# Kernel optimization log

Measured on AMD Instinct MI355X. Metric: run time of the kernel, lower is better.

## Reference

```python
import jax, jax.numpy as jnp
import numpy as np

DIM = 2048
NUM_HEADS = 16
HEAD_DIM = DIM // NUM_HEADS
HIDDEN = 4 * DIM
EPS = 1e-6


def rmsnorm(x, w):
    # Faithful to source: weight * (x * dim**-0.5 / sqrt(mean(x^2) + eps))
    scale = DIM ** -0.5
    norm = jnp.sqrt(jnp.mean(x * x, axis=-1, keepdims=True) + EPS)
    return w * (x * scale / norm)


def setup_inputs() -> dict:
    key = jax.random.key(0)
    ks = jax.random.split(key, 10)
    def init(k, shape, fan_in):
        return jax.random.normal(k, shape, dtype=jnp.float32) * (fan_in ** -0.5)
    return {
        "x": jax.random.normal(ks[0], (2, 2048, DIM), dtype=jnp.float32),
        "norm1_w": jnp.ones((DIM,), dtype=jnp.float32),
        "wq": init(ks[1], (DIM, DIM), DIM),
        "wk": init(ks[2], (HEAD_DIM, DIM), DIM),
        "wv": init(ks[3], (HEAD_DIM, DIM), DIM),
        "wo": init(ks[4], (DIM, DIM), DIM),
        "norm2_w": jnp.ones((DIM,), dtype=jnp.float32),
        "w1": init(ks[5], (HIDDEN, DIM), DIM),
        "w2": init(ks[6], (DIM, HIDDEN), HIDDEN),
        "w3": init(ks[7], (HIDDEN, DIM), DIM),
    }


def reference(x, norm1_w, wq, wk, wv, wo, norm2_w, w1, w2, w3):
    B, S, _ = x.shape
    # --- Multi-Query Attention (pre-norm) ---
    h = rmsnorm(x, norm1_w)
    q = h @ wq.T                                  # [B,S,D]
    k = h @ wk.T                                  # [B,S,hd] (shared across heads)
    v = h @ wv.T                                  # [B,S,hd]
    q = q.reshape(B, S, NUM_HEADS, HEAD_DIM)
    # scores: q @ k^T / sqrt(hd); k is broadcast (repeated) across heads
    scores = jnp.einsum('bshd,btd->bhst', q, k) / (HEAD_DIM ** 0.5)  # [B,H,S,S]
    probs = jax.nn.softmax(scores, axis=-1)
    attn = jnp.einsum('bhst,btd->bshd', probs, v).reshape(B, S, DIM)
    x = x + attn @ wo.T
    # --- SwiGLU FFN (pre-norm) ---
    h = rmsnorm(x, norm2_w)
    ffn = (jax.nn.silu(h @ w1.T) * (h @ w3.T)) @ w2.T
    return x + ffn
```

## Files before the change

kernel.cpp:

```cpp
#include <hip/hip_runtime.h>
#include <hip/hip_bf16.h>

typedef __attribute__((ext_vector_type(4))) float f32x4;
typedef __attribute__((ext_vector_type(8))) short s16x8;
typedef __attribute__((ext_vector_type(4))) short s16x4;
typedef __attribute__((ext_vector_type(2))) short s16x2;

#define MFMA_BF16 __builtin_amdgcn_mfma_f32_16x16x32_bf16

__device__ inline short f2bf(float f) {
  unsigned u = __float_as_uint(f);
  u = (u + 0x7FFFu + ((u >> 16) & 1u)) >> 16;
  return (short)u;
}
__device__ inline float bf2f(short s) {
  return __uint_as_float(((unsigned)(unsigned short)s) << 16);
}

#define DPPF(x, ctrl) __int_as_float(__builtin_amdgcn_update_dpp( \
    __float_as_int(x), __float_as_int(x), ctrl, 0xF, 0xF, false))
__device__ inline float rowmax16(float x) {
  x = fmaxf(x, DPPF(x, 0xB1));
  x = fmaxf(x, DPPF(x, 0x4E));
  x = fmaxf(x, DPPF(x, 0x124));
  x = fmaxf(x, DPPF(x, 0x128));
  return x;
}
__device__ inline float rowsum16(float x) {
  x += DPPF(x, 0xB1);
  x += DPPF(x, 0x4E);
  x += DPPF(x, 0x124);
  x += DPPF(x, 0x128);
  return x;
}

__global__ __launch_bounds__(256) void cvt_kernel(
    const float* __restrict__ in, short* __restrict__ out, int n, float scale)
{
  int idx = (blockIdx.x * 256 + threadIdx.x) * 8;
  if (idx >= n) return;
  f32x4 a = *(const f32x4*)(in + idx);
  f32x4 b = *(const f32x4*)(in + idx + 4);
  s16x8 o;
  #pragma unroll
  for (int j = 0; j < 4; ++j) { o[j] = f2bf(a[j] * scale); o[4 + j] = f2bf(b[j] * scale); }
  *(s16x8*)(out + idx) = o;
}

__global__ __launch_bounds__(256) void rmsnorm_kernel(
    const float* __restrict__ x, const float* __restrict__ w, short* __restrict__ out)
{
  size_t row = blockIdx.x;
  const float* xr = x + row * 2048;
  int base = threadIdx.x * 8;
  f32x4 a = *(const f32x4*)(xr + base);
  f32x4 b = *(const f32x4*)(xr + base + 4);
  float ss = a[0]*a[0] + a[1]*a[1] + a[2]*a[2] + a[3]*a[3]
           + b[0]*b[0] + b[1]*b[1] + b[2]*b[2] + b[3]*b[3];
  #pragma unroll
  for (int off = 1; off < 64; off <<= 1) ss += __shfl_xor(ss, off, 64);
  __shared__ float red[4];
  if ((threadIdx.x & 63) == 0) red[threadIdx.x >> 6] = ss;
  __syncthreads();
  float tot = red[0] + red[1] + red[2] + red[3];
  float rn = rsqrtf(tot * (1.0f / 2048.0f) + 1e-6f) * 0.022097086912079608f;
  f32x4 wa = *(const f32x4*)(w + base);
  f32x4 wb = *(const f32x4*)(w + base + 4);
  s16x8 o;
  #pragma unroll
  for (int j = 0; j < 4; ++j) {
    o[j]     = f2bf(a[j] * wa[j] * rn);
    o[4 + j] = f2bf(b[j] * wb[j] * rn);
  }
  *(s16x8*)(out + row * 2048 + base) = o;
}

template <int MODE>
__global__ __launch_bounds__(256, 2) void gemm_bt_kernel(
    const short* __restrict__ A, const short* __restrict__ B,
    void* __restrict__ Cv, const float* __restrict__ resid,
    int M, int N, int K)
{
  __shared__ short As[128 * 32];
  __shared__ short Bs[128 * 32];
  int tid = threadIdx.x;
  int lane = tid & 63;
  int w = tid >> 6;
  int r = lane & 15, g = lane >> 4;
  int wr = w >> 1, wc = w & 1;
  size_t row0 = (size_t)blockIdx.y * 128;
  size_t col0 = (size_t)blockIdx.x * 128;

  f32x4 acc[4][4];
  #pragma unroll
  for (int i = 0; i < 4; ++i)
    #pragma unroll
    for (int j = 0; j < 4; ++j) acc[i][j] = (f32x4){0.f, 0.f, 0.f, 0.f};

  const short* Ablk = A + row0 * K;
  const short* Bblk = B + col0 * K;
  int arow = tid >> 2;
  int akk = (tid & 3) << 3;

  for (int k0 = 0; k0 < K; k0 += 32) {
    #pragma unroll
    for (int i = 0; i < 2; ++i) {
      int chunk = i * 256 + tid;
      int rr = i * 64 + arow;
      __builtin_amdgcn_global_load_lds(
          (const __attribute__((address_space(1))) unsigned int*)(Ablk + (size_t)rr * K + k0 + akk),
          (__attribute__((address_space(3))) unsigned int*)(&As[chunk * 8]), 16, 0, 0);
      __builtin_amdgcn_global_load_lds(
          (const __attribute__((address_space(1))) unsigned int*)(Bblk + (size_t)rr * K + k0 + akk),
          (__attribute__((address_space(3))) unsigned int*)(&Bs[chunk * 8]), 16, 0, 0);
    }
    __syncthreads();
    s16x8 af[4], bfr[4];
    #pragma unroll
    for (int mm = 0; mm < 4; ++mm)
      af[mm] = *(const s16x8*)(&As[(wr * 64 + mm * 16 + r) * 32 + g * 8]);
    #pragma unroll
    for (int nn = 0; nn < 4; ++nn)
      bfr[nn] = *(const s16x8*)(&Bs[(wc * 64 + nn * 16 + r) * 32 + g * 8]);
    #pragma unroll
    for (int mm = 0; mm < 4; ++mm)
      #pragma unroll
      for (int nn = 0; nn < 4; ++nn)
        acc[mm][nn] = MFMA_BF16(af[mm], bfr[nn], acc[mm][nn], 0, 0, 0);
    __syncthreads();
  }

  #pragma unroll
  for (int mm = 0; mm < 4; ++mm) {
    #pragma unroll
    for (int nn = 0; nn < 4; ++nn) {
      #pragma unroll
      for (int j = 0; j < 4; ++j) {
        size_t rr = row0 + wr * 64 + mm * 16 + g * 4 + j;
        size_t cc = col0 + wc * 64 + nn * 16 + r;
        size_t idx = rr * (size_t)N + cc;
        if constexpr (MODE == 0) {
          ((short*)Cv)[idx] = f2bf(acc[mm][nn][j]);
        } else if constexpr (MODE == 1) {
          ((float*)Cv)[idx] = acc[mm][nn][j] + resid[idx];
        } else {
          short* gp = (short*)Cv;
          float gv = bf2f(gp[idx]);
          float sg = gv / (1.0f + __expf(-gv));
          gp[idx] = f2bf(sg * acc[mm][nn][j]);
        }
      }
    }
  }
}


#define STAGEA2(T)                                                             \
  _Pragma("unroll")                                                            \
  for (int i = 0; i < 4; ++i) {                                                \
    int lc = i * 512 + tid;                                                    \
    int rw = lc >> 3, ch = lc & 7;                                             \
    __builtin_amdgcn_global_load_lds(                                          \
        (const __attribute__((address_space(1))) unsigned int*)                \
            (Ablk + (size_t)rw * K + (T) * 64 + ((ch ^ (rw & 7)) << 3)),       \
        (__attribute__((address_space(3))) unsigned int*)                      \
            (&As[(T) & 1][lc * 8]), 16, 0, 0);                                 \
  }

#define STAGEB2(T)                                                             \
  _Pragma("unroll")                                                            \
  for (int i = 0; i < BLOADS2; ++i) {                                          \
    int lc = i * 512 + tid;                                                    \
    int rw = lc >> 3, ch = lc & 7;                                             \
    __builtin_amdgcn_global_load_lds(                                          \
        (const __attribute__((address_space(1))) unsigned int*)                \
            (Bblk + (size_t)rw * K + (T) * 64 + ((ch ^ (rw & 7)) << 3)),       \
        (__attribute__((address_space(3))) unsigned int*)                      \
            (&Bs[(T) & 1][lc * 8]), 16, 0, 0);                                 \
  }

#define LDALL(D, KS)                                                           \
  _Pragma("unroll")                                                            \
  for (int mi = 0; mi < 8; ++mi) {                                             \
    int rowa = wr * 128 + mi * 16 + r;                                         \
    aR[mi] = *(const s16x8*)(&As[D][rowa * 64 + ((((KS) * 4 + g) ^ (rowa & 7)) << 3)]); \
  }                                                                            \
  _Pragma("unroll")                                                            \
  for (int ni = 0; ni < NREP; ++ni) {                                          \
    int rowb = wc * WN + ni * 16 + r;                                          \
    bR[ni] = *(const s16x8*)(&Bs[D][rowb * 64 + ((((KS) * 4 + g) ^ (rowb & 7)) << 3)]); \
  }

#define MFALL                                                                  \
  __builtin_amdgcn_s_setprio(1);                                               \
  _Pragma("unroll")                                                            \
  for (int mi = 0; mi < 8; ++mi)                                               \
    _Pragma("unroll")                                                          \
    for (int ni = 0; ni < NREP; ++ni)                                          \
      acc[mi][ni] = MFMA_BF16(aR[mi], bR[ni], acc[mi][ni], 0, 0, 0);           \
  __builtin_amdgcn_s_setprio(0);

#define BAR __builtin_amdgcn_s_barrier()
#define VM0 asm volatile("s_waitcnt vmcnt(0)" ::: "memory")

template <int BN, int MODE>
__global__ __launch_bounds__(512, 2) void gemm2p_kernel(
    const short* __restrict__ A, const short* __restrict__ B,
    void* __restrict__ Cv, const float* __restrict__ resid,
    int M, int N, int K)
{
  constexpr int BLOADS2 = BN / 64;
  constexpr int WN = BN / 4;
  constexpr int NREP = WN / 16;
  __shared__ short As[2][256 * 64];
  __shared__ short Bs[2][BN * 64];

  int tid = threadIdx.x;
  int lane = tid & 63;
  int w = tid >> 6;
  int r = lane & 15, g = lane >> 4;
  int wr = w >> 2, wc = w & 3;

  int nwg = gridDim.x * gridDim.y;
  int orig = blockIdx.y * gridDim.x + blockIdx.x;
  int swz = (orig & 7) * (nwg >> 3) + (orig >> 3);
  int bx = swz % gridDim.x, by = swz / gridDim.x;
  size_t row0 = (size_t)by * 256;
  size_t col0 = (size_t)bx * BN;

  const short* Ablk = A + row0 * K;
  const short* Bblk = B + col0 * K;

  f32x4 acc[8][NREP];
  #pragma unroll
  for (int i = 0; i < 8; ++i)
    #pragma unroll
    for (int j = 0; j < NREP; ++j) acc[i][j] = (f32x4){0.f, 0.f, 0.f, 0.f};

  s16x8 aR[8], bR[NREP];
  int NT = K >> 6;

  STAGEA2(0); STAGEB2(0);
  VM0;
  BAR;

  for (int t = 0; t < NT; ++t) {
    int d = t & 1;
    bool nl = (t < NT - 1);
    if (nl) { STAGEA2(t + 1); STAGEB2(t + 1); }
    LDALL(d, 0);
    BAR;
    MFALL;
    BAR;
    LDALL(d, 1);
    VM0;
    BAR;
    MFALL;
    BAR;
  }

  #pragma unroll
  for (int mi = 0; mi < 8; ++mi) {
    #pragma unroll
    for (int ni = 0; ni < NREP; ++ni) {
      #pragma unroll
      for (int j = 0; j < 4; ++j) {
        size_t rr = row0 + wr * 128 + mi * 16 + g * 4 + j;
        size_t cc = col0 + wc * WN + ni * 16 + r;
        size_t idx = rr * (size_t)N + cc;
        if constexpr (MODE == 0) {
          ((short*)Cv)[idx] = f2bf(acc[mi][ni][j]);
        } else if constexpr (MODE == 1) {
          ((float*)Cv)[idx] = acc[mi][ni][j] + resid[idx];
        } else {
          short* gp = (short*)Cv;
          float gv = bf2f(gp[idx]);
          float sg = gv / (1.0f + __expf(-gv));
          gp[idx] = f2bf(sg * acc[mi][ni][j]);
        }
      }
    }
  }
}

__global__ __launch_bounds__(256) void transpose_v_kernel(
    const short* __restrict__ kv, short* __restrict__ vt)
{
  __shared__ short t[64][65];
  int b = blockIdx.z;
  int s0 = blockIdx.x * 64;
  int d0 = blockIdx.y * 64;
  int tid = threadIdx.x;
  #pragma unroll
  for (int i = 0; i < 16; ++i) {
    int e = i * 256 + tid;
    int sr = e >> 6, dc = e & 63;
    t[sr][dc] = kv[(size_t)(b * 2048 + s0 + sr) * 256 + 128 + d0 + dc];
  }
  __syncthreads();
  #pragma unroll
  for (int i = 0; i < 16; ++i) {
    int e = i * 256 + tid;
    int dr = e >> 6, sc = e & 63;
    vt[(size_t)b * 128 * 2048 + (size_t)(d0 + dr) * 2048 + s0 + sc] = t[sc][dr];
  }
}

__global__ __launch_bounds__(256, 2) void attn_kernel(
    const short* __restrict__ q, const short* __restrict__ kv,
    const short* __restrict__ vt, short* __restrict__ out)
{
  const int S = 2048;
  int tid = threadIdx.x;
  int w = tid >> 6;
  int lane = tid & 63;
  int r = lane & 15, g = lane >> 4;
  int h = blockIdx.y, b = blockIdx.z;
  int qrow0 = blockIdx.x * 128 + w * 32;

  __shared__ short Ks[2][4096];
  __shared__ short Vs[2][4096];
  __shared__ short Ps[4][32][40];

  const short* kvsrc = kv + (size_t)b * S * 256;
  const short* vsrc  = vt + (size_t)b * 128 * S;

  const short* qbase = q + ((size_t)(b * S + qrow0 + r)) * 2048 + h * 128;
  s16x8 qa[2][4];
  #pragma unroll
  for (int gq = 0; gq < 2; ++gq)
    #pragma unroll
    for (int dc = 0; dc < 4; ++dc)
      qa[gq][dc] = *(const s16x8*)(qbase + gq * 16 * 2048 + dc * 32 + g * 8);

  f32x4 o[2][8];
  #pragma unroll
  for (int gq = 0; gq < 2; ++gq)
    #pragma unroll
    for (int dt = 0; dt < 8; ++dt) o[gq][dt] = (f32x4){0.f, 0.f, 0.f, 0.f};
  float m[2][4], l[2][4];
  #pragma unroll
  for (int gq = 0; gq < 2; ++gq)
    #pragma unroll
    for (int j = 0; j < 4; ++j) { m[gq][j] = -1e30f; l[gq][j] = 0.f; }

#define STAGE(KVT, BSEL)                                                        \
  {                                                                             \
    int kv0s = (KVT) * 32;                                                      \
    _Pragma("unroll")                                                           \
    for (int i = 0; i < 2; ++i) {                                               \
      int c = w * 64 + lane + i * 256;                                          \
      int krow = c >> 4, kcp = c & 15;                                          \
      __builtin_amdgcn_global_load_lds(                                         \
          (const __attribute__((address_space(1))) unsigned int*)               \
              (kvsrc + (size_t)(kv0s + krow) * 256 + ((kcp ^ (krow & 7)) << 3)),\
          (__attribute__((address_space(3))) unsigned int*)(&Ks[BSEL][c * 8]),  \
          16, 0, 0);                                                            \
      int vrow = c >> 2, vcp = c & 3;                                           \
      __builtin_amdgcn_global_load_lds(                                         \
          (const __attribute__((address_space(1))) unsigned int*)               \
              (vsrc + (size_t)vrow * S + kv0s + ((vcp ^ (vrow & 3)) << 3)),     \
          (__attribute__((address_space(3))) unsigned int*)(&Vs[BSEL][c * 8]),  \
          16, 0, 0);                                                            \
    }                                                                           \
  }

  STAGE(0, 0);
  __syncthreads();

  for (int it = 0; it < 64; ++it) {
    int cur = it & 1;
    if (it < 63) STAGE(it + 1, cur ^ 1);

    s16x8 kc0[4], kc1[4], vb[8];
    #pragma unroll
    for (int dc = 0; dc < 4; ++dc) {
      kc0[dc] = *(const s16x8*)(&Ks[cur][r * 128 + (((dc * 4 + g) ^ (r & 7)) << 3)]);
      kc1[dc] = *(const s16x8*)(&Ks[cur][(16 + r) * 128 + (((dc * 4 + g) ^ (r & 7)) << 3)]);
    }
    #pragma unroll
    for (int dt = 0; dt < 8; ++dt)
      vb[dt] = *(const s16x8*)(&Vs[cur][(dt * 16 + r) * 32 + ((g ^ (r & 3)) << 3)]);

    f32x4 sc0[2], sc1[2];
    #pragma unroll
    for (int gq = 0; gq < 2; ++gq) { sc0[gq] = (f32x4){0.f,0.f,0.f,0.f}; sc1[gq] = (f32x4){0.f,0.f,0.f,0.f}; }
    __builtin_amdgcn_s_setprio(1);
    #pragma unroll
    for (int dc = 0; dc < 4; ++dc) {
      #pragma unroll
      for (int gq = 0; gq < 2; ++gq) {
        sc0[gq] = MFMA_BF16(qa[gq][dc], kc0[dc], sc0[gq], 0, 0, 0);
        sc1[gq] = MFMA_BF16(qa[gq][dc], kc1[dc], sc1[gq], 0, 0, 0);
      }
    }
    __builtin_amdgcn_s_setprio(0);

    float p0[2][4], p1[2][4];
    #pragma unroll
    for (int gq = 0; gq < 2; ++gq) {
      float mx[4];
      #pragma unroll
      for (int j = 0; j < 4; ++j) mx[j] = rowmax16(fmaxf(sc0[gq][j], sc1[gq][j]));
      bool nd = (mx[0] > m[gq][0] + 8.f) | (mx[1] > m[gq][1] + 8.f)
              | (mx[2] > m[gq][2] + 8.f) | (mx[3] > m[gq][3] + 8.f);
      if (__any(nd)) {
        #pragma unroll
        for (int j = 0; j < 4; ++j) {
          float mn = fmaxf(m[gq][j], mx[j]);
          float alpha = __expf(m[gq][j] - mn);
          m[gq][j] = mn;
          l[gq][j] *= alpha;
          #pragma unroll
          for (int dt = 0; dt < 8; ++dt) o[gq][dt][j] *= alpha;
        }
      }
      #pragma unroll
      for (int j = 0; j < 4; ++j) {
        p0[gq][j] = __expf(sc0[gq][j] - m[gq][j]);
        p1[gq][j] = __expf(sc1[gq][j] - m[gq][j]);
        l[gq][j] += p0[gq][j] + p1[gq][j];
      }
      #pragma unroll
      for (int j = 0; j < 4; ++j) {
        Ps[w][gq * 16 + g * 4 + j][r]      = f2bf(p0[gq][j]);
        Ps[w][gq * 16 + g * 4 + j][16 + r] = f2bf(p1[gq][j]);
      }
    }
    asm volatile("s_waitcnt lgkmcnt(0)" ::: "memory");
    __builtin_amdgcn_sched_barrier(0);
    s16x8 pa0 = *(const s16x8*)(&Ps[w][r][g * 8]);
    s16x8 pa1 = *(const s16x8*)(&Ps[w][16 + r][g * 8]);
    __builtin_amdgcn_s_setprio(1);
    #pragma unroll
    for (int dt = 0; dt < 8; ++dt) {
      o[0][dt] = MFMA_BF16(pa0, vb[dt], o[0][dt], 0, 0, 0);
      o[1][dt] = MFMA_BF16(pa1, vb[dt], o[1][dt], 0, 0, 0);
    }
    __builtin_amdgcn_s_setprio(0);
    __syncthreads();
  }

  #pragma unroll
  for (int gq = 0; gq < 2; ++gq) {
    float linv[4];
    #pragma unroll
    for (int j = 0; j < 4; ++j) linv[j] = 1.0f / rowsum16(l[gq][j]);
    short* ob = out + ((size_t)(b * S + qrow0 + gq * 16)) * 2048 + h * 128;
    #pragma unroll
    for (int dt = 0; dt < 8; ++dt)
      #pragma unroll
      for (int j = 0; j < 4; ++j)
        ob[(size_t)(g * 4 + j) * 2048 + dt * 16 + r] = f2bf(o[gq][dt][j] * linv[j]);
  }
#undef STAGE
}

extern "C" void kernel_launch(void* const* d_in, const int* in_sizes, int n_in,
                              void* d_out, int out_size, void* d_ws, size_t ws_size,
                              hipStream_t stream) {
  const float* x   = (const float*)d_in[0];
  const float* n1w = (const float*)d_in[1];
  const float* wq  = (const float*)d_in[2];
  const float* wk  = (const float*)d_in[3];
  const float* wv  = (const float*)d_in[4];
  const float* wo  = (const float*)d_in[5];
  const float* n2w = (const float*)d_in[6];
  const float* w1  = (const float*)d_in[7];
  const float* w2  = (const float*)d_in[8];
  const float* w3  = (const float*)d_in[9];
  float* out = (float*)d_out;
  char* ws = (char*)d_ws;
  const size_t MB = 1ull << 20;
  short* wqb  = (short*)(ws);
  short* wob  = (short*)(ws + 8 * MB);
  short* w1b  = (short*)(ws + 16 * MB);
  short* w2b  = (short*)(ws + 48 * MB);
  short* w3b  = (short*)(ws + 80 * MB);
  short* wkvb = (short*)(ws + 112 * MB);
  short* h1   = (short*)(ws + 113 * MB);
  short* gbuf = (short*)(ws + 129 * MB);
  short* qb   = (short*)(ws + 129 * MB);
  short* kvb  = (short*)(ws + 145 * MB);
  short* vtb  = (short*)(ws + 147 * MB);

  const float qscale = 0.08838834764831845f;
  cvt_kernel<<<2048, 256, 0, stream>>>(wq, wqb, 4194304, qscale);
  cvt_kernel<<<128,  256, 0, stream>>>(wk, wkvb, 262144, 1.0f);
  cvt_kernel<<<128,  256, 0, stream>>>(wv, wkvb + 262144, 262144, 1.0f);
  cvt_kernel<<<2048, 256, 0, stream>>>(wo, wob, 4194304, 1.0f);
  cvt_kernel<<<8192, 256, 0, stream>>>(w1, w1b, 16777216, 1.0f);
  cvt_kernel<<<8192, 256, 0, stream>>>(w2, w2b, 16777216, 1.0f);
  cvt_kernel<<<8192, 256, 0, stream>>>(w3, w3b, 16777216, 1.0f);

  rmsnorm_kernel<<<4096, 256, 0, stream>>>(x, n1w, h1);
  gemm2p_kernel<128, 0><<<dim3(16, 16), 512, 0, stream>>>(h1, wqb, qb, nullptr, 4096, 2048, 2048);
  gemm_bt_kernel<0><<<dim3(2, 32), 256, 0, stream>>>(h1, wkvb, kvb, nullptr, 4096, 256, 2048);
  transpose_v_kernel<<<dim3(32, 2, 2), 256, 0, stream>>>(kvb, vtb);
  attn_kernel<<<dim3(16, 16, 2), 256, 0, stream>>>(qb, kvb, vtb, h1);
  gemm2p_kernel<128, 1><<<dim3(16, 16), 512, 0, stream>>>(h1, wob, out, x, 4096, 2048, 2048);
  rmsnorm_kernel<<<4096, 256, 0, stream>>>(out, n2w, h1);
  gemm2p_kernel<256, 0><<<dim3(32, 16), 512, 0, stream>>>(h1, w1b, gbuf, nullptr, 4096, 8192, 2048);
  gemm2p_kernel<256, 2><<<dim3(32, 16), 512, 0, stream>>>(h1, w3b, gbuf, nullptr, 4096, 8192, 2048);
  gemm2p_kernel<128, 1><<<dim3(16, 16), 512, 0, stream>>>(gbuf, w2b, out, out, 4096, 2048, 8192);
}
```

Before: 967.6 us.

## Replace 256-row 512-thread GEMM with 128x128 256-thread tile kernel

Swaps the large-tile GEMM (256xBN tile, 8 waves) for a 128x128 tile with 4 waves, each computing 64x64, and launches more workgroups for every projection. The main loop now issues the next tile's loads, then waits with a partial vmcnt and a single barrier before both k-substeps, instead of four barriers per iteration. Smaller tiles raise the workgroup count and cut per-iteration synchronisation, but they lower arithmetic intensity and increase global/LDS traffic per FLOP.

```diff
diff --git a/kernel.cpp b/kernel.cpp
--- a/kernel.cpp
+++ b/kernel.cpp
@@ -155,10 +155,10 @@
 }
 
 
-#define STAGEA2(T)                                                             \
+#define STAGEA1(T)                                                             \
   _Pragma("unroll")                                                            \
   for (int i = 0; i < 4; ++i) {                                                \
-    int lc = i * 512 + tid;                                                    \
+    int lc = i * 256 + tid;                                                    \
     int rw = lc >> 3, ch = lc & 7;                                             \
     __builtin_amdgcn_global_load_lds(                                          \
         (const __attribute__((address_space(1))) unsigned int*)                \
@@ -167,10 +167,10 @@
             (&As[(T) & 1][lc * 8]), 16, 0, 0);                                 \
   }
 
-#define STAGEB2(T)                                                             \
+#define STAGEB1(T)                                                             \
   _Pragma("unroll")                                                            \
-  for (int i = 0; i < BLOADS2; ++i) {                                          \
-    int lc = i * 512 + tid;                                                    \
+  for (int i = 0; i < 4; ++i) {                                                \
+    int lc = i * 256 + tid;                                                    \
     int rw = lc >> 3, ch = lc & 7;                                             \
     __builtin_amdgcn_global_load_lds(                                          \
         (const __attribute__((address_space(1))) unsigned int*)                \
@@ -179,94 +179,90 @@
             (&Bs[(T) & 1][lc * 8]), 16, 0, 0);                                 \
   }
 
-#define LDALL(D, KS)                                                           \
+#define LDK(KS, D)                                                             \
   _Pragma("unroll")                                                            \
-  for (int mi = 0; mi < 8; ++mi) {                                             \
-    int rowa = wr * 128 + mi * 16 + r;                                         \
-    aR[mi] = *(const s16x8*)(&As[D][rowa * 64 + ((((KS) * 4 + g) ^ (rowa & 7)) << 3)]); \
+  for (int mi = 0; mi < 4; ++mi) {                                             \
+    int rowa = wr * 64 + mi * 16 + r;                                          \
+    aR[mi] = *(const s16x8*)(&As[D][rowa * 64 + (((KS) * 4 + g) ^ (rowa & 7)) * 8]); \
   }                                                                            \
   _Pragma("unroll")                                                            \
-  for (int ni = 0; ni < NREP; ++ni) {                                          \
-    int rowb = wc * WN + ni * 16 + r;                                          \
-    bR[ni] = *(const s16x8*)(&Bs[D][rowb * 64 + ((((KS) * 4 + g) ^ (rowb & 7)) << 3)]); \
-  }
-
-#define MFALL                                                                  \
+  for (int ni = 0; ni < 4; ++ni) {                                             \
+    int rowb = wc * 64 + ni * 16 + r;                                          \
+    bR[ni] = *(const s16x8*)(&Bs[D][rowb * 64 + (((KS) * 4 + g) ^ (rowb & 7)) * 8]); \
+  }
+
+#define MF16A                                                                  \
   __builtin_amdgcn_s_setprio(1);                                               \
   _Pragma("unroll")                                                            \
-  for (int mi = 0; mi < 8; ++mi)                                               \
+  for (int mi = 0; mi < 4; ++mi)                                               \
     _Pragma("unroll")                                                          \
-    for (int ni = 0; ni < NREP; ++ni)                                          \
+    for (int ni = 0; ni < 4; ++ni)                                             \
       acc[mi][ni] = MFMA_BF16(aR[mi], bR[ni], acc[mi][ni], 0, 0, 0);           \
   __builtin_amdgcn_s_setprio(0);
 
 #define BAR __builtin_amdgcn_s_barrier()
-#define VM0 asm volatile("s_waitcnt vmcnt(0)" ::: "memory")
-
-template <int BN, int MODE>
-__global__ __launch_bounds__(512, 2) void gemm2p_kernel(
+
+template <int MODE>
+__global__ __launch_bounds__(256, 2) void gemm128_kernel(
     const short* __restrict__ A, const short* __restrict__ B,
     void* __restrict__ Cv, const float* __restrict__ resid,
     int M, int N, int K)
 {
-  constexpr int BLOADS2 = BN / 64;
-  constexpr int WN = BN / 4;
-  constexpr int NREP = WN / 16;
-  __shared__ short As[2][256 * 64];
-  __shared__ short Bs[2][BN * 64];
+  __shared__ short As[2][128 * 64];
+  __shared__ short Bs[2][128 * 64];
 
   int tid = threadIdx.x;
   int lane = tid & 63;
   int w = tid >> 6;
   int r = lane & 15, g = lane >> 4;
-  int wr = w >> 2, wc = w & 3;
+  int wr = w >> 1, wc = w & 1;
 
   int nwg = gridDim.x * gridDim.y;
   int orig = blockIdx.y * gridDim.x + blockIdx.x;
   int swz = (orig & 7) * (nwg >> 3) + (orig >> 3);
   int bx = swz % gridDim.x, by = swz / gridDim.x;
-  size_t row0 = (size_t)by * 256;
-  size_t col0 = (size_t)bx * BN;
+  size_t row0 = (size_t)by * 128;
+  size_t col0 = (size_t)bx * 128;
 
   const short* Ablk = A + row0 * K;
   const short* Bblk = B + col0 * K;
 
-  f32x4 acc[8][NREP];
-  #pragma unroll
-  for (int i = 0; i < 8; ++i)
-    #pragma unroll
-    for (int j = 0; j < NREP; ++j) acc[i][j] = (f32x4){0.f, 0.f, 0.f, 0.f};
-
-  s16x8 aR[8], bR[NREP];
+  f32x4 acc[4][4];
+  #pragma unroll
+  for (int i = 0; i < 4; ++i)
+    #pragma unroll
+    for (int j = 0; j < 4; ++j) acc[i][j] = (f32x4){0.f, 0.f, 0.f, 0.f};
+
+  s16x8 aR[4], bR[4];
   int NT = K >> 6;
 
-  STAGEA2(0); STAGEB2(0);
-  VM0;
-  BAR;
+  STAGEA1(0); STAGEB1(0);
 
   for (int t = 0; t < NT; ++t) {
     int d = t & 1;
     bool nl = (t < NT - 1);
-    if (nl) { STAGEA2(t + 1); STAGEB2(t + 1); }
-    LDALL(d, 0);
+    if (nl) {
+      STAGEA1(t + 1); STAGEB1(t + 1);
+      asm volatile("s_waitcnt vmcnt(8)" ::: "memory");
+    } else {
+      asm volatile("s_waitcnt vmcnt(0)" ::: "memory");
+    }
     BAR;
-    MFALL;
+    LDK(0, d);
+    MF16A;
+    LDK(1, d);
+    MF16A;
     BAR;
-    LDALL(d, 1);
-    VM0;
-    BAR;
-    MFALL;
-    BAR;
-  }
-
-  #pragma unroll
-  for (int mi = 0; mi < 8; ++mi) {
-    #pragma unroll
-    for (int ni = 0; ni < NREP; ++ni) {
+  }
+
+  #pragma unroll
+  for (int mi = 0; mi < 4; ++mi) {
+    #pragma unroll
+    for (int ni = 0; ni < 4; ++ni) {
       #pragma unroll
       for (int j = 0; j < 4; ++j) {
-        size_t rr = row0 + wr * 128 + mi * 16 + g * 4 + j;
-        size_t cc = col0 + wc * WN + ni * 16 + r;
+        size_t rr = row0 + wr * 64 + mi * 16 + g * 4 + j;
+        size_t cc = col0 + wc * 64 + ni * 16 + r;
         size_t idx = rr * (size_t)N + cc;
         if constexpr (MODE == 0) {
           ((short*)Cv)[idx] = f2bf(acc[mi][ni][j]);
@@ -494,13 +490,13 @@
   cvt_kernel<<<8192, 256, 0, stream>>>(w3, w3b, 16777216, 1.0f);
 
   rmsnorm_kernel<<<4096, 256, 0, stream>>>(x, n1w, h1);
-  gemm2p_kernel<128, 0><<<dim3(16, 16), 512, 0, stream>>>(h1, wqb, qb, nullptr, 4096, 2048, 2048);
+  gemm128_kernel<0><<<dim3(16, 32), 256, 0, stream>>>(h1, wqb, qb, nullptr, 4096, 2048, 2048);
   gemm_bt_kernel<0><<<dim3(2, 32), 256, 0, stream>>>(h1, wkvb, kvb, nullptr, 4096, 256, 2048);
   transpose_v_kernel<<<dim3(32, 2, 2), 256, 0, stream>>>(kvb, vtb);
   attn_kernel<<<dim3(16, 16, 2), 256, 0, stream>>>(qb, kvb, vtb, h1);
-  gemm2p_kernel<128, 1><<<dim3(16, 16), 512, 0, stream>>>(h1, wob, out, x, 4096, 2048, 2048);
+  gemm128_kernel<1><<<dim3(16, 32), 256, 0, stream>>>(h1, wob, out, x, 4096, 2048, 2048);
   rmsnorm_kernel<<<4096, 256, 0, stream>>>(out, n2w, h1);
-  gemm2p_kernel<256, 0><<<dim3(32, 16), 512, 0, stream>>>(h1, w1b, gbuf, nullptr, 4096, 8192, 2048);
-  gemm2p_kernel<256, 2><<<dim3(32, 16), 512, 0, stream>>>(h1, w3b, gbuf, nullptr, 4096, 8192, 2048);
-  gemm2p_kernel<128, 1><<<dim3(16, 16), 512, 0, stream>>>(gbuf, w2b, out, out, 4096, 2048, 8192);
-}
+  gemm128_kernel<0><<<dim3(64, 32), 256, 0, stream>>>(h1, w1b, gbuf, nullptr, 4096, 8192, 2048);
+  gemm128_kernel<2><<<dim3(64, 32), 256, 0, stream>>>(h1, w3b, gbuf, nullptr, 4096, 8192, 2048);
+  gemm128_kernel<1><<<dim3(16, 32), 256, 0, stream>>>(gbuf, w2b, out, out, 4096, 2048, 8192);
+}
```

After: 890.7 us. -7.9%, faster.
